# Kernel optimization log

Measured on AMD Instinct MI355X. Metric: run time of the kernel, lower is better.

Reference implementation:

```python
import jax, jax.numpy as jnp
import numpy as np

D_MODEL = 1024
NUM_HEADS = 16
HEAD_DIM = D_MODEL // NUM_HEADS  # 64
ROPE_THETA = 10000.0
BATCH = 2
SEQ = 2048
NEG_INF = -1e30


def setup_inputs() -> dict:
    key = jax.random.key(0)
    ks = jax.random.split(key, 6)
    std = 1.0 / np.sqrt(D_MODEL)
    x = jax.random.normal(ks[0], (BATCH, SEQ, D_MODEL), dtype=jnp.float32)
    wq = jax.random.normal(ks[1], (D_MODEL, D_MODEL), dtype=jnp.float32) * std
    wk = jax.random.normal(ks[2], (D_MODEL, D_MODEL), dtype=jnp.float32) * std
    wv = jax.random.normal(ks[3], (D_MODEL, D_MODEL), dtype=jnp.float32) * std
    wo = jax.random.normal(ks[4], (D_MODEL, D_MODEL), dtype=jnp.float32) * std
    token_positions = jnp.broadcast_to(jnp.arange(SEQ, dtype=jnp.int32)[None, :], (BATCH, SEQ))
    return {"x": x, "token_positions": token_positions, "wq": wq, "wk": wk, "wv": wv, "wo": wo}


def _apply_rope(t, token_positions):
    # t: (B, H, S, head_dim), token_positions: (B, S)
    half = HEAD_DIM // 2
    inv_freq = 1.0 / (ROPE_THETA ** (2.0 * jnp.arange(half, dtype=jnp.float32) / HEAD_DIM))
    angles = token_positions.astype(jnp.float32)[..., None] * inv_freq  # (B, S, half)
    cos = jnp.cos(angles)[:, None, :, :]  # (B, 1, S, half)
    sin = jnp.sin(angles)[:, None, :, :]
    tp = t.reshape(*t.shape[:-1], half, 2)  # interleaved pairs
    x1, x2 = tp[..., 0], tp[..., 1]
    r1 = x1 * cos - x2 * sin
    r2 = x1 * sin + x2 * cos
    return jnp.stack([r1, r2], axis=-1).reshape(t.shape)


def reference(x, token_positions, wq, wk, wv, wo):
    B, S, D = x.shape
    H, hd = NUM_HEADS, HEAD_DIM
    # projections (Linear: y = x @ W.T, no bias)
    q = (x @ wq.T).reshape(B, S, H, hd).transpose(0, 2, 1, 3)  # (B, H, S, hd)
    k = (x @ wk.T).reshape(B, S, H, hd).transpose(0, 2, 1, 3)
    v = (x @ wv.T).reshape(B, S, H, hd).transpose(0, 2, 1, 3)
    # RoPE on Q, K
    q = _apply_rope(q, token_positions)
    k = _apply_rope(k, token_positions)
    # causal scaled dot-product attention
    scores = jnp.einsum("bhqd,bhkd->bhqk", q, k) / jnp.sqrt(jnp.float32(hd))
    mask = jnp.tril(jnp.ones((S, S), dtype=bool))
    scores = jnp.where(mask, scores, NEG_INF)
    probs = jax.nn.softmax(scores, axis=-1)
    attn = jnp.einsum("bhqk,bhkd->bhqd", probs, v)  # (B, H, S, hd)
    attn = attn.transpose(0, 2, 1, 3).reshape(B, S, D)
    return attn @ wo.T
```

## Files before the change

kernel.cpp:

```cpp
#include <hip/hip_runtime.h>
#include <stdint.h>
#include <math.h>

#define SEQ 2048
#define NH 16
#define DM 1024

typedef __bf16 bf16x8 __attribute__((ext_vector_type(8)));
typedef __bf16 bf16x2 __attribute__((ext_vector_type(2)));
typedef short s16x4 __attribute__((ext_vector_type(4)));
typedef short s16x8 __attribute__((ext_vector_type(8)));
typedef float f32x4 __attribute__((ext_vector_type(4)));
typedef float f32x2 __attribute__((ext_vector_type(2)));

#define ASM_VMCNT0  asm volatile("s_waitcnt vmcnt(0)" ::: "memory")
#define ASM_BARRIER asm volatile("s_barrier" ::: "memory")

__device__ __forceinline__ unsigned short f2bf(float f) {
  union { float f; unsigned u; } v; v.f = f;
  unsigned r = v.u + 0x7fffu + ((v.u >> 16) & 1u);
  return (unsigned short)(r >> 16);
}
__device__ __forceinline__ unsigned pk2(float a, float b) {
  f32x2 v = {a, b};
  bf16x2 r = __builtin_convertvector(v, bf16x2);
  union { bf16x2 h; unsigned u; } c; c.h = r;
  return c.u;
}
__device__ __forceinline__ void load_lds16(const void* g, void* l) {
  __builtin_amdgcn_global_load_lds((__attribute__((address_space(1))) void*)g,
                                   (__attribute__((address_space(3))) void*)l,
                                   16, 0, 0);
}

__global__ void cvt_all(const float* __restrict__ x, const float* __restrict__ wq,
                        const float* __restrict__ wk, const float* __restrict__ wv,
                        const float* __restrict__ wo, unsigned short* __restrict__ ws) {
  const int i = blockIdx.x * blockDim.x + threadIdx.x;
  const int off = i * 4;
  const float* src;
  unsigned short* dst;
  if (off < 4194304) {
    src = x + off;  dst = ws + off;
  } else {
    const int r = off - 4194304;
    const int w = r >> 20, o = r & 1048575;
    const float* tabs[4] = {wq, wk, wv, wo};
    src = tabs[w] + o;  dst = ws + 4194304 + (w << 20) + o;
  }
  const float4 v = *(const float4*)src;
  uint2 u;
  u.x = pk2(v.x, v.y);
  u.y = pk2(v.z, v.w);
  *(uint2*)dst = u;
}

__launch_bounds__(256, 3)
__global__ void gemm_qkv(const unsigned short* __restrict__ X,
                         const unsigned short* __restrict__ W3,
                         unsigned short* __restrict__ Qr,
                         unsigned short* __restrict__ Kr,
                         unsigned short* __restrict__ Vt,
                         const int* __restrict__ tp) {
  __shared__ __align__(16) char smem[32768];

  const int t = threadIdx.x;
  const int lane = t & 63, wave = t >> 6;
  const int quad = lane >> 4, l16 = lane & 15;
  const int m0 = blockIdx.y * 128, n0 = blockIdx.x * 128;
  const int wm = (wave >> 1) * 64, wn = (wave & 1) * 64;

  f32x4 acc[4][4];
#pragma unroll
  for (int i = 0; i < 4; i++)
#pragma unroll
    for (int j = 0; j < 4; j++) { acc[i][j][0]=0.f; acc[i][j][1]=0.f; acc[i][j][2]=0.f; acc[i][j][3]=0.f; }

  const int rr = t >> 2;
  const int cc = (t & 3) * 8;

#define QKV_STAGE(bufidx, k0_) do {                                               \
    char* a_ = smem + (bufidx) * 8192;                                            \
    char* b_ = smem + 16384 + (bufidx) * 8192;                                    \
    _Pragma("unroll")                                                             \
    for (int i_ = 0; i_ < 2; i_++) {                                              \
      load_lds16(X  + (uint64_t)(m0 + i_ * 64 + rr) * 1024 + (k0_) + cc,          \
                 a_ + i_ * 4096 + wave * 1024);                                   \
      load_lds16(W3 + (uint64_t)(n0 + i_ * 64 + rr) * 1024 + (k0_) + cc,          \
                 b_ + i_ * 4096 + wave * 1024);                                   \
    }                                                                             \
  } while (0)

  QKV_STAGE(0, 0);

  for (int k0 = 0; k0 < 1024; k0 += 32) {
    const int buf = (k0 >> 5) & 1;
    ASM_VMCNT0;
    ASM_BARRIER;
    if (k0 + 32 < 1024) QKV_STAGE(buf ^ 1, k0 + 32);
    char* As = smem + buf * 8192;
    char* Bs = smem + 16384 + buf * 8192;

    bf16x8 af[4], bfr[4];
#pragma unroll
    for (int i = 0; i < 4; i++) {
      af[i]  = *(const bf16x8*)(As + (wm + i * 16 + l16) * 64 + quad * 16);
      bfr[i] = *(const bf16x8*)(Bs + (wn + i * 16 + l16) * 64 + quad * 16);
    }
#pragma unroll
    for (int i = 0; i < 4; i++)
#pragma unroll
      for (int j = 0; j < 4; j++)
        acc[i][j] = __builtin_amdgcn_mfma_f32_16x16x32_bf16(af[i], bfr[j], acc[i][j], 0, 0, 0);
  }
#undef QKV_STAGE

  if (n0 < 2048) {
    unsigned short* dst = (n0 < 1024) ? Qr : Kr;
    float fr[4]; int dd[4], hh[4];
#pragma unroll
    for (int j = 0; j < 4; j++) {
      const int n = n0 + wn + j * 16 + l16;
      dd[j] = n & 63;
      hh[j] = (n & 1023) >> 6;
      fr[j] = __builtin_amdgcn_exp2f(-0.20762050594f * (float)(dd[j] & ~1)) * 0.15915494309f;
    }
    const float sgnodd = (l16 & 1) ? 1.f : -1.f;
#pragma unroll
    for (int i = 0; i < 4; i++) {
#pragma unroll
      for (int r = 0; r < 4; r++) {
        const int m = m0 + wm + i * 16 + quad * 4 + r;
        const int s = m & 2047, b = m >> 11;
        const float posf = (float)tp[m];
#pragma unroll
        for (int j = 0; j < 4; j++) {
          const float v = acc[i][j][r];
          const float p = __shfl_xor(v, 1);
          float rev = posf * fr[j];
          rev -= floorf(rev);
          float sn, cs;
          asm("v_sin_f32 %0, %1" : "=v"(sn) : "v"(rev));
          asm("v_cos_f32 %0, %1" : "=v"(cs) : "v"(rev));
          const float rv = fmaf(v, cs, p * sn * sgnodd);
          dst[((uint64_t)((b * NH + hh[j]) * SEQ + s)) * 64 + dd[j]] = f2bf(rv);
        }
      }
    }
  } else {
#pragma unroll
    for (int i = 0; i < 4; i++) {
      const int m = m0 + wm + i * 16 + quad * 4;
      const int s = m & 2047, b = m >> 11;
      const int sl = s & 63;
      const int qv = (sl >> 2) & 3, nv = sl >> 4;
      const int g = (s & ~63) + qv * 16 + (nv >> 1) * 8 + (nv & 1) * 4;
#pragma unroll
      for (int j = 0; j < 4; j++) {
        const int n = n0 - 2048 + wn + j * 16 + l16;
        const int h = n >> 6, d = n & 63;
        uint2 w;
        w.x = pk2(acc[i][j][0], acc[i][j][1]);
        w.y = pk2(acc[i][j][2], acc[i][j][3]);
        *(uint2*)(Vt + ((uint64_t)((b * NH + h) * 64 + d)) * SEQ + g) = w;
      }
    }
  }
}

__launch_bounds__(256, 2)
__global__ void gemm_ao(const unsigned short* __restrict__ A,
                        const unsigned short* __restrict__ B,
                        float* __restrict__ C) {
  __shared__ __align__(16) char smem[32768];

  const int t = threadIdx.x;
  const int lane = t & 63, wave = t >> 6;
  const int quad = lane >> 4, l16 = lane & 15;
  const int m0 = blockIdx.y * 128, n0 = blockIdx.x * 128;
  const int wm = (wave >> 1) * 64, wn = (wave & 1) * 64;

  f32x4 acc[4][4];
#pragma unroll
  for (int i = 0; i < 4; i++)
#pragma unroll
    for (int j = 0; j < 4; j++) { acc[i][j][0]=0.f; acc[i][j][1]=0.f; acc[i][j][2]=0.f; acc[i][j][3]=0.f; }

  const int rr = t >> 2;
  const int cc = (t & 3) * 8;

#define AO_STAGE(bufidx, k0_) do {                                               \
    char* a_ = smem + (bufidx) * 8192;                                            \
    char* b_ = smem + 16384 + (bufidx) * 8192;                                    \
    _Pragma("unroll")                                                             \
    for (int i_ = 0; i_ < 2; i_++) {                                              \
      load_lds16(A + (uint64_t)(m0 + i_ * 64 + rr) * 1024 + (k0_) + cc,           \
                 a_ + i_ * 4096 + wave * 1024);                                   \
      load_lds16(B + (uint64_t)(n0 + i_ * 64 + rr) * 1024 + (k0_) + cc,           \
                 b_ + i_ * 4096 + wave * 1024);                                   \
    }                                                                             \
  } while (0)

  AO_STAGE(0, 0);

  for (int k0 = 0; k0 < 1024; k0 += 32) {
    const int buf = (k0 >> 5) & 1;
    ASM_VMCNT0;
    ASM_BARRIER;
    if (k0 + 32 < 1024) AO_STAGE(buf ^ 1, k0 + 32);
    char* As = smem + buf * 8192;
    char* Bs = smem + 16384 + buf * 8192;

    bf16x8 af[4], bfr[4];
#pragma unroll
    for (int i = 0; i < 4; i++) {
      af[i]  = *(const bf16x8*)(As + (wm + i * 16 + l16) * 64 + quad * 16);
      bfr[i] = *(const bf16x8*)(Bs + (wn + i * 16 + l16) * 64 + quad * 16);
    }
#pragma unroll
    for (int i = 0; i < 4; i++)
#pragma unroll
      for (int j = 0; j < 4; j++)
        acc[i][j] = __builtin_amdgcn_mfma_f32_16x16x32_bf16(af[i], bfr[j], acc[i][j], 0, 0, 0);
  }
#undef AO_STAGE

#pragma unroll
  for (int i = 0; i < 4; i++)
#pragma unroll
    for (int j = 0; j < 4; j++)
#pragma unroll
      for (int r = 0; r < 4; r++) {
        const int m = m0 + wm + i * 16 + quad * 4 + r;
        const int n = n0 + wn + j * 16 + l16;
        C[(uint64_t)m * DM + n] = acc[i][j][r];
      }
}

__launch_bounds__(512, 2)
__global__ void flash_attn(const unsigned short* __restrict__ Q,
                           const unsigned short* __restrict__ K,
                           const unsigned short* __restrict__ Vt,
                           unsigned short* __restrict__ Oa) {
  __shared__ __align__(16) char smem[32768];

  const int t = threadIdx.x;
  const int lane = t & 63, wave = t >> 6;
  const int quad = lane >> 4, l16 = lane & 15;
  const int lid = blockIdx.x;
  const int bh = lid & 31;
  const int a = lid >> 5;
  const uint64_t base = (uint64_t)bh * (SEQ * 64);
  const int qb0 = a * 128, qb1 = (15 - a) * 128;
  const int n0 = 2 * a + 2;
  const int qg0 = qb0 + wave * 16 + l16;
  const int qg1 = qb1 + wave * 16 + l16;
  const int b = bh >> 4, h = bh & 15;

  bf16x8 qf0[2], qf1[2];
  {
    const unsigned short* qp = Q + base + (uint64_t)qg0 * 64 + quad * 8;
    qf0[0] = *(const bf16x8*)qp;  qf0[1] = *(const bf16x8*)(qp + 32);
    const unsigned short* qq = Q + base + (uint64_t)qg1 * 64 + quad * 8;
    qf1[0] = *(const bf16x8*)qq;  qf1[1] = *(const bf16x8*)(qq + 32);
  }

  f32x4 o[4];
#pragma unroll
  for (int i = 0; i < 4; i++) { o[i][0]=0.f; o[i][1]=0.f; o[i][2]=0.f; o[i][3]=0.f; }
  float lI = 0.f;

  const int srow = wave * 8 + (lane >> 3);
  const int sc = ((lane & 7) ^ ((lane >> 3) & 7)) * 8;
  const int swz = (l16 & 7);

#define STAGE(bufidx, kb_) do {                                                   \
    load_lds16(K  + base + (uint64_t)((kb_) + srow) * 64 + sc,                    \
               smem + (bufidx) * 8192 + wave * 1024);                             \
    load_lds16(Vt + base + (uint64_t)srow * SEQ + (kb_) + sc,                     \
               smem + 16384 + (bufidx) * 8192 + wave * 1024);                     \
  } while (0)

  STAGE(0, 0);

  const float c1 = 0.18033688011f;

  for (int it = 0; it < 34; it++) {
    const bool ph1 = it >= n0;
    const int kb = (ph1 ? it - n0 : it) * 64;
    const int buf = it & 1;
    ASM_VMCNT0;
    ASM_BARRIER;
    if (it + 1 < 34) {
      const int itn = it + 1;
      const int kbn = ((itn >= n0) ? itn - n0 : itn) * 64;
      STAGE(buf ^ 1, kbn);
    }
    char* ks = smem + buf * 8192;
    char* vs = smem + 16384 + buf * 8192;

    const bf16x8* qf = ph1 ? qf1 : qf0;
    const int qg = ph1 ? qg1 : qg0;
    const int qb = ph1 ? qb1 : qb0;
    int nbmax = ((qb + wave * 16 + 15 - kb) >> 4) + 1;
    nbmax = nbmax > 4 ? 4 : (nbmax < 0 ? 0 : nbmax);
    const bool diag = (kb + 63) > (qb + wave * 16);

    f32x4 sf[4];
    float ls = 0.f;
#pragma unroll
    for (int nb = 0; nb < 4; nb++) {
      if (nb < nbmax) {
        f32x4 s; s[0]=0.f; s[1]=0.f; s[2]=0.f; s[3]=0.f;
#pragma unroll
        for (int kk = 0; kk < 2; kk++) {
          bf16x8 kfr = *(const bf16x8*)(ks + (nb * 16 + l16) * 128 + (((kk * 4 + quad) ^ swz) * 16));
          s = __builtin_amdgcn_mfma_f32_16x16x32_bf16(kfr, qf[kk], s, 0, 0, 0);
        }
        if (diag) {
#pragma unroll
          for (int r = 0; r < 4; r++) {
            const int key = kb + nb * 16 + quad * 4 + r;
            const float p = (key <= qg) ? __builtin_amdgcn_exp2f(s[r] * c1) : 0.f;
            sf[nb][r] = p;  ls += p;
          }
        } else {
#pragma unroll
          for (int r = 0; r < 4; r++) {
            const float p = __builtin_amdgcn_exp2f(s[r] * c1);
            sf[nb][r] = p;  ls += p;
          }
        }
      }
    }
    lI += ls;

#pragma unroll
    for (int np = 0; np < 2; np++) {
      if (2 * np < nbmax) {
        union { uint2 u; s16x4 h; } p0;
        p0.u.x = pk2(sf[2 * np][0], sf[2 * np][1]);
        p0.u.y = pk2(sf[2 * np][2], sf[2 * np][3]);
        const bool hi = (2 * np + 1 < nbmax);
        union { uint2 u; s16x4 h; } p1;
        if (hi) {
          p1.u.x = pk2(sf[2 * np + 1][0], sf[2 * np + 1][1]);
          p1.u.y = pk2(sf[2 * np + 1][2], sf[2 * np + 1][3]);
        }
#pragma unroll
        for (int db = 0; db < 4; db++) {
          s16x8 vv = *(const s16x8*)(vs + (db * 16 + l16) * 128 +
                                     (((quad * 2 + np) ^ swz) * 16));
          s16x4 vlo = __builtin_shufflevector(vv, vv, 0, 1, 2, 3);
          o[db] = __builtin_amdgcn_mfma_f32_16x16x16bf16_1k(vlo, p0.h, o[db], 0, 0, 0);
          if (hi) {
            s16x4 vhi = __builtin_shufflevector(vv, vv, 4, 5, 6, 7);
            o[db] = __builtin_amdgcn_mfma_f32_16x16x16bf16_1k(vhi, p1.h, o[db], 0, 0, 0);
          }
        }
      }
    }

    if (it == n0 - 1) {
      float lr = lI;
      lr += __shfl_xor(lr, 16);
      lr += __shfl_xor(lr, 32);
      const float invl = 1.0f / lr;
      unsigned short* orow = Oa + ((uint64_t)(b * SEQ + qg0)) * DM + h * 64 + quad * 4;
#pragma unroll
      for (int db = 0; db < 4; db++) {
        uint2 w;
        w.x = pk2(o[db][0] * invl, o[db][1] * invl);
        w.y = pk2(o[db][2] * invl, o[db][3] * invl);
        *(uint2*)(orow + db * 16) = w;
        o[db][0]=0.f; o[db][1]=0.f; o[db][2]=0.f; o[db][3]=0.f;
      }
      lI = 0.f;
    }
  }
#undef STAGE

  float lr = lI;
  lr += __shfl_xor(lr, 16);
  lr += __shfl_xor(lr, 32);
  const float invl = 1.0f / lr;
  unsigned short* orow = Oa + ((uint64_t)(b * SEQ + qg1)) * DM + h * 64 + quad * 4;
#pragma unroll
  for (int db = 0; db < 4; db++) {
    uint2 w;
    w.x = pk2(o[db][0] * invl, o[db][1] * invl);
    w.y = pk2(o[db][2] * invl, o[db][3] * invl);
    *(uint2*)(orow + db * 16) = w;
  }
}

extern "C" void kernel_launch(void* const* d_in, const int* in_sizes, int n_in,
                              void* d_out, int out_size, void* d_ws, size_t ws_size,
                              hipStream_t stream) {
  const float* x  = (const float*)d_in[0];
  const int* tp   = (const int*)d_in[1];
  const float* wq = (const float*)d_in[2];
  const float* wk = (const float*)d_in[3];
  const float* wv = (const float*)d_in[4];
  const float* wo = (const float*)d_in[5];
  float* out = (float*)d_out;

  unsigned short* ws = (unsigned short*)d_ws;
  unsigned short* xb  = ws;
  unsigned short* w3b = ws + 4194304;
  unsigned short* wob = ws + 7340032;
  unsigned short* Qr  = ws + 8388608;
  unsigned short* Kr  = ws + 12582912;
  unsigned short* Vt  = ws + 16777216;
  unsigned short* At  = ws + 20971520;

  cvt_all<<<8192, 256, 0, stream>>>(x, wq, wk, wv, wo, ws);
  gemm_qkv<<<dim3(24, 32), 256, 0, stream>>>(xb, w3b, Qr, Kr, Vt, tp);
  flash_attn<<<256, 512, 0, stream>>>(Qr, Kr, Vt, At);
  gemm_ao<<<dim3(8, 32), 256, 0, stream>>>(At, wob, out);
}
```

Before: 178.3 us.

## Split waves into two groups processing paired causal q-tiles concurrently

After: 183.0 us. 1.03x slower.

```diff
diff --git a/kernel.cpp b/kernel.cpp
--- a/kernel.cpp
+++ b/kernel.cpp
@@ -242,156 +242,165 @@
                            const unsigned short* __restrict__ K,
                            const unsigned short* __restrict__ Vt,
                            unsigned short* __restrict__ Oa) {
-  __shared__ __align__(16) char smem[32768];
+  __shared__ __align__(16) char smem[65536];
 
   const int t = threadIdx.x;
   const int lane = t & 63, wave = t >> 6;
   const int quad = lane >> 4, l16 = lane & 15;
+  const int g = wave >> 2, wv = wave & 3;
   const int lid = blockIdx.x;
   const int bh = lid & 31;
   const int a = lid >> 5;
   const uint64_t base = (uint64_t)bh * (SEQ * 64);
-  const int qb0 = a * 128, qb1 = (15 - a) * 128;
-  const int n0 = 2 * a + 2;
-  const int qg0 = qb0 + wave * 16 + l16;
-  const int qg1 = qb1 + wave * 16 + l16;
+  const int qb = (g ? (15 - a) : a) * 128;
+  const int ng0 = 2 * a + 2, ng1 = 32 - 2 * a;
+  const int ngMy = g ? ng1 : ng0;
+  const int qlo = qb + wv * 32;
+  const int qg0 = qlo + l16;
+  const int qg1 = qlo + 16 + l16;
   const int b = bh >> 4, h = bh & 15;
 
-  bf16x8 qf0[2], qf1[2];
+  bf16x8 qf[2][2];
   {
-    const unsigned short* qp = Q + base + (uint64_t)qg0 * 64 + quad * 8;
-    qf0[0] = *(const bf16x8*)qp;  qf0[1] = *(const bf16x8*)(qp + 32);
-    const unsigned short* qq = Q + base + (uint64_t)qg1 * 64 + quad * 8;
-    qf1[0] = *(const bf16x8*)qq;  qf1[1] = *(const bf16x8*)(qq + 32);
-  }
-
-  f32x4 o[4];
-#pragma unroll
-  for (int i = 0; i < 4; i++) { o[i][0]=0.f; o[i][1]=0.f; o[i][2]=0.f; o[i][3]=0.f; }
-  float lI = 0.f;
+    const unsigned short* qp0 = Q + base + (uint64_t)qg0 * 64 + quad * 8;
+    qf[0][0] = *(const bf16x8*)qp0;  qf[0][1] = *(const bf16x8*)(qp0 + 32);
+    const unsigned short* qp1 = Q + base + (uint64_t)qg1 * 64 + quad * 8;
+    qf[1][0] = *(const bf16x8*)qp1;  qf[1][1] = *(const bf16x8*)(qp1 + 32);
+  }
+
+  f32x4 o0[4], o1[4];
+#pragma unroll
+  for (int i = 0; i < 4; i++) {
+    o0[i][0]=0.f; o0[i][1]=0.f; o0[i][2]=0.f; o0[i][3]=0.f;
+    o1[i][0]=0.f; o1[i][1]=0.f; o1[i][2]=0.f; o1[i][3]=0.f;
+  }
+  float lI0 = 0.f, lI1 = 0.f;
 
   const int srow = wave * 8 + (lane >> 3);
   const int sc = ((lane & 7) ^ ((lane >> 3) & 7)) * 8;
   const int swz = (l16 & 7);
 
-#define STAGE(bufidx, kb_) do {                                                   \
+#define STAGE(gg, bufidx, kb_) do {                                               \
     load_lds16(K  + base + (uint64_t)((kb_) + srow) * 64 + sc,                    \
-               smem + (bufidx) * 8192 + wave * 1024);                             \
+               smem + (gg) * 32768 + (bufidx) * 16384 + wave * 1024);             \
     load_lds16(Vt + base + (uint64_t)srow * SEQ + (kb_) + sc,                     \
-               smem + 16384 + (bufidx) * 8192 + wave * 1024);                     \
+               smem + (gg) * 32768 + (bufidx) * 16384 + 8192 + wave * 1024);      \
   } while (0)
 
-  STAGE(0, 0);
+  STAGE(0, 0, 0);
+  STAGE(1, 0, 0);
 
   const float c1 = 0.18033688011f;
-
-  for (int it = 0; it < 34; it++) {
-    const bool ph1 = it >= n0;
-    const int kb = (ph1 ? it - n0 : it) * 64;
+  const int nIt = ng1;
+
+  for (int it = 0; it < nIt; it++) {
     const int buf = it & 1;
     ASM_VMCNT0;
     ASM_BARRIER;
-    if (it + 1 < 34) {
-      const int itn = it + 1;
-      const int kbn = ((itn >= n0) ? itn - n0 : itn) * 64;
-      STAGE(buf ^ 1, kbn);
-    }
-    char* ks = smem + buf * 8192;
-    char* vs = smem + 16384 + buf * 8192;
-
-    const bf16x8* qf = ph1 ? qf1 : qf0;
-    const int qg = ph1 ? qg1 : qg0;
-    const int qb = ph1 ? qb1 : qb0;
-    int nbmax = ((qb + wave * 16 + 15 - kb) >> 4) + 1;
-    nbmax = nbmax > 4 ? 4 : (nbmax < 0 ? 0 : nbmax);
-    const bool diag = (kb + 63) > (qb + wave * 16);
-
-    f32x4 sf[4];
-    float ls = 0.f;
-#pragma unroll
-    for (int nb = 0; nb < 4; nb++) {
-      if (nb < nbmax) {
-        f32x4 s; s[0]=0.f; s[1]=0.f; s[2]=0.f; s[3]=0.f;
-#pragma unroll
-        for (int kk = 0; kk < 2; kk++) {
-          bf16x8 kfr = *(const bf16x8*)(ks + (nb * 16 + l16) * 128 + (((kk * 4 + quad) ^ swz) * 16));
-          s = __builtin_amdgcn_mfma_f32_16x16x32_bf16(kfr, qf[kk], s, 0, 0, 0);
-        }
-        if (diag) {
-#pragma unroll
-          for (int r = 0; r < 4; r++) {
-            const int key = kb + nb * 16 + quad * 4 + r;
-            const float p = (key <= qg) ? __builtin_amdgcn_exp2f(s[r] * c1) : 0.f;
-            sf[nb][r] = p;  ls += p;
+    const int itn = it + 1;
+    if (itn < ng0) STAGE(0, itn & 1, itn * 64);
+    if (itn < ng1) STAGE(1, itn & 1, itn * 64);
+
+    if (it < ngMy) {
+      const int kb = it * 64;
+      char* ks = smem + g * 32768 + buf * 16384;
+      char* vs = ks + 8192;
+
+      int nbmax = ((qlo + 31 - kb) >> 4) + 1;
+      nbmax = nbmax > 4 ? 4 : (nbmax < 0 ? 0 : nbmax);
+      const bool diag = (kb + 63) > qlo;
+
+      f32x4 sf0[4], sf1[4];
+      float ls0 = 0.f, ls1 = 0.f;
+#pragma unroll
+      for (int nb = 0; nb < 4; nb++) {
+        if (nb < nbmax) {
+          f32x4 s0; s0[0]=0.f; s0[1]=0.f; s0[2]=0.f; s0[3]=0.f;
+          f32x4 s1; s1[0]=0.f; s1[1]=0.f; s1[2]=0.f; s1[3]=0.f;
+#pragma unroll
+          for (int kk = 0; kk < 2; kk++) {
+            bf16x8 kfr = *(const bf16x8*)(ks + (nb * 16 + l16) * 128 + (((kk * 4 + quad) ^ swz) * 16));
+            s0 = __builtin_amdgcn_mfma_f32_16x16x32_bf16(kfr, qf[0][kk], s0, 0, 0, 0);
+            s1 = __builtin_amdgcn_mfma_f32_16x16x32_bf16(kfr, qf[1][kk], s1, 0, 0, 0);
           }
-        } else {
-#pragma unroll
-          for (int r = 0; r < 4; r++) {
-            const float p = __builtin_amdgcn_exp2f(s[r] * c1);
-            sf[nb][r] = p;  ls += p;
+          if (diag) {
+#pragma unroll
+            for (int r = 0; r < 4; r++) {
+              const int key = kb + nb * 16 + quad * 4 + r;
+              const float p0 = (key <= qg0) ? __builtin_amdgcn_exp2f(s0[r] * c1) : 0.f;
+              sf0[nb][r] = p0;  ls0 += p0;
+              const float p1 = (key <= qg1) ? __builtin_amdgcn_exp2f(s1[r] * c1) : 0.f;
+              sf1[nb][r] = p1;  ls1 += p1;
+            }
+          } else {
+#pragma unroll
+            for (int r = 0; r < 4; r++) {
+              const float p0 = __builtin_amdgcn_exp2f(s0[r] * c1);
+              sf0[nb][r] = p0;  ls0 += p0;
+              const float p1 = __builtin_amdgcn_exp2f(s1[r] * c1);
+              sf1[nb][r] = p1;  ls1 += p1;
+            }
           }
         }
       }
-    }
-    lI += ls;
-
-#pragma unroll
-    for (int np = 0; np < 2; np++) {
-      if (2 * np < nbmax) {
-        union { uint2 u; s16x4 h; } p0;
-        p0.u.x = pk2(sf[2 * np][0], sf[2 * np][1]);
-        p0.u.y = pk2(sf[2 * np][2], sf[2 * np][3]);
-        const bool hi = (2 * np + 1 < nbmax);
-        union { uint2 u; s16x4 h; } p1;
-        if (hi) {
-          p1.u.x = pk2(sf[2 * np + 1][0], sf[2 * np + 1][1]);
-          p1.u.y = pk2(sf[2 * np + 1][2], sf[2 * np + 1][3]);
-        }
-#pragma unroll
-        for (int db = 0; db < 4; db++) {
-          s16x8 vv = *(const s16x8*)(vs + (db * 16 + l16) * 128 +
-                                     (((quad * 2 + np) ^ swz) * 16));
-          s16x4 vlo = __builtin_shufflevector(vv, vv, 0, 1, 2, 3);
-          o[db] = __builtin_amdgcn_mfma_f32_16x16x16bf16_1k(vlo, p0.h, o[db], 0, 0, 0);
+      lI0 += ls0;  lI1 += ls1;
+
+#pragma unroll
+      for (int np = 0; np < 2; np++) {
+        if (2 * np < nbmax) {
+          union { uint2 u; s16x4 h; } a0, b0, a1, b1;
+          a0.u.x = pk2(sf0[2 * np][0], sf0[2 * np][1]);
+          a0.u.y = pk2(sf0[2 * np][2], sf0[2 * np][3]);
+          b0.u.x = pk2(sf1[2 * np][0], sf1[2 * np][1]);
+          b0.u.y = pk2(sf1[2 * np][2], sf1[2 * np][3]);
+          const bool hi = (2 * np + 1 < nbmax);
           if (hi) {
-            s16x4 vhi = __builtin_shufflevector(vv, vv, 4, 5, 6, 7);
-            o[db] = __builtin_amdgcn_mfma_f32_16x16x16bf16_1k(vhi, p1.h, o[db], 0, 0, 0);
+            a1.u.x = pk2(sf0[2 * np + 1][0], sf0[2 * np + 1][1]);
+            a1.u.y = pk2(sf0[2 * np + 1][2], sf0[2 * np + 1][3]);
+            b1.u.x = pk2(sf1[2 * np + 1][0], sf1[2 * np + 1][1]);
+            b1.u.y = pk2(sf1[2 * np + 1][2], sf1[2 * np + 1][3]);
+          }
+#pragma unroll
+          for (int db = 0; db < 4; db++) {
+            s16x8 vv = *(const s16x8*)(vs + (db * 16 + l16) * 128 +
+                                       (((quad * 2 + np) ^ swz) * 16));
+            s16x4 vlo = __builtin_shufflevector(vv, vv, 0, 1, 2, 3);
+            o0[db] = __builtin_amdgcn_mfma_f32_16x16x16bf16_1k(vlo, a0.h, o0[db], 0, 0, 0);
+            o1[db] = __builtin_amdgcn_mfma_f32_16x16x16bf16_1k(vlo, b0.h, o1[db], 0, 0, 0);
+            if (hi) {
+              s16x4 vhi = __builtin_shufflevector(vv, vv, 4, 5, 6, 7);
+              o0[db] = __builtin_amdgcn_mfma_f32_16x16x16bf16_1k(vhi, a1.h, o0[db], 0, 0, 0);
+              o1[db] = __builtin_amdgcn_mfma_f32_16x16x16bf16_1k(vhi, b1.h, o1[db], 0, 0, 0);
+            }
           }
         }
       }
-    }
-
-    if (it == n0 - 1) {
-      float lr = lI;
-      lr += __shfl_xor(lr, 16);
-      lr += __shfl_xor(lr, 32);
-      const float invl = 1.0f / lr;
-      unsigned short* orow = Oa + ((uint64_t)(b * SEQ + qg0)) * DM + h * 64 + quad * 4;
-#pragma unroll
-      for (int db = 0; db < 4; db++) {
-        uint2 w;
-        w.x = pk2(o[db][0] * invl, o[db][1] * invl);
-        w.y = pk2(o[db][2] * invl, o[db][3] * invl);
-        *(uint2*)(orow + db * 16) = w;
-        o[db][0]=0.f; o[db][1]=0.f; o[db][2]=0.f; o[db][3]=0.f;
-      }
-      lI = 0.f;
+
+      if (it == ngMy - 1) {
+        float lr0 = lI0;
+        lr0 += __shfl_xor(lr0, 16);
+        lr0 += __shfl_xor(lr0, 32);
+        const float il0 = 1.0f / lr0;
+        float lr1 = lI1;
+        lr1 += __shfl_xor(lr1, 16);
+        lr1 += __shfl_xor(lr1, 32);
+        const float il1 = 1.0f / lr1;
+        unsigned short* p0r = Oa + ((uint64_t)(b * SEQ + qg0)) * DM + h * 64 + quad * 4;
+        unsigned short* p1r = Oa + ((uint64_t)(b * SEQ + qg1)) * DM + h * 64 + quad * 4;
+#pragma unroll
+        for (int db = 0; db < 4; db++) {
+          uint2 w;
+          w.x = pk2(o0[db][0] * il0, o0[db][1] * il0);
+          w.y = pk2(o0[db][2] * il0, o0[db][3] * il0);
+          *(uint2*)(p0r + db * 16) = w;
+          w.x = pk2(o1[db][0] * il1, o1[db][1] * il1);
+          w.y = pk2(o1[db][2] * il1, o1[db][3] * il1);
+          *(uint2*)(p1r + db * 16) = w;
+        }
+      }
     }
   }
 #undef STAGE
-
-  float lr = lI;
-  lr += __shfl_xor(lr, 16);
-  lr += __shfl_xor(lr, 32);
-  const float invl = 1.0f / lr;
-  unsigned short* orow = Oa + ((uint64_t)(b * SEQ + qg1)) * DM + h * 64 + quad * 4;
-#pragma unroll
-  for (int db = 0; db < 4; db++) {
-    uint2 w;
-    w.x = pk2(o[db][0] * invl, o[db][1] * invl);
-    w.y = pk2(o[db][2] * invl, o[db][3] * invl);
-    *(uint2*)(orow + db * 16) = w;
-  }
 }
 
 extern "C" void kernel_launch(void* const* d_in, const int* in_sizes, int n_in,
```

## Split flash attention into 64-row query tiles, heaviest-first, with 256-thread blocks

Applied to the files above, without the earlier changes.

After: 174.2 us. -2.3%, faster.

```diff
diff --git a/kernel.cpp b/kernel.cpp
--- a/kernel.cpp
+++ b/kernel.cpp
@@ -237,7 +237,7 @@
       }
 }
 
-__launch_bounds__(512, 2)
+__launch_bounds__(256, 4)
 __global__ void flash_attn(const unsigned short* __restrict__ Q,
                            const unsigned short* __restrict__ K,
                            const unsigned short* __restrict__ Vt,
@@ -245,24 +245,21 @@
   __shared__ __align__(16) char smem[32768];
 
   const int t = threadIdx.x;
-  const int lane = t & 63, wave = t >> 6;
+  const int lane = t & 63, wid = t >> 6;
   const int quad = lane >> 4, l16 = lane & 15;
-  const int lid = blockIdx.x;
-  const int bh = lid & 31;
-  const int a = lid >> 5;
+  const int u = blockIdx.x;
+  const int tq = 31 - (u >> 5);
+  const int bh = u & 31;
   const uint64_t base = (uint64_t)bh * (SEQ * 64);
-  const int qb0 = a * 128, qb1 = (15 - a) * 128;
-  const int n0 = 2 * a + 2;
-  const int qg0 = qb0 + wave * 16 + l16;
-  const int qg1 = qb1 + wave * 16 + l16;
+  const int qb = tq * 64;
+  const int ng = tq + 1;
+  const int qg = qb + wid * 16 + l16;
   const int b = bh >> 4, h = bh & 15;
 
-  bf16x8 qf0[2], qf1[2];
+  bf16x8 qf[2];
   {
-    const unsigned short* qp = Q + base + (uint64_t)qg0 * 64 + quad * 8;
-    qf0[0] = *(const bf16x8*)qp;  qf0[1] = *(const bf16x8*)(qp + 32);
-    const unsigned short* qq = Q + base + (uint64_t)qg1 * 64 + quad * 8;
-    qf1[0] = *(const bf16x8*)qq;  qf1[1] = *(const bf16x8*)(qq + 32);
+    const unsigned short* qp = Q + base + (uint64_t)qg * 64 + quad * 8;
+    qf[0] = *(const bf16x8*)qp;  qf[1] = *(const bf16x8*)(qp + 32);
   }
 
   f32x4 o[4];
@@ -270,41 +267,37 @@
   for (int i = 0; i < 4; i++) { o[i][0]=0.f; o[i][1]=0.f; o[i][2]=0.f; o[i][3]=0.f; }
   float lI = 0.f;
 
-  const int srow = wave * 8 + (lane >> 3);
-  const int sc = ((lane & 7) ^ ((lane >> 3) & 7)) * 8;
+  const int sr8 = lane >> 3;
+  const int sc = ((lane & 7) ^ sr8) * 8;
   const int swz = (l16 & 7);
 
 #define STAGE(bufidx, kb_) do {                                                   \
-    load_lds16(K  + base + (uint64_t)((kb_) + srow) * 64 + sc,                    \
-               smem + (bufidx) * 8192 + wave * 1024);                             \
-    load_lds16(Vt + base + (uint64_t)srow * SEQ + (kb_) + sc,                     \
-               smem + 16384 + (bufidx) * 8192 + wave * 1024);                     \
+    _Pragma("unroll")                                                             \
+    for (int i_ = 0; i_ < 2; i_++) {                                              \
+      const int r_ = wid * 16 + i_ * 8 + sr8;                                     \
+      load_lds16(K  + base + (uint64_t)((kb_) + r_) * 64 + sc,                    \
+                 smem + (bufidx) * 8192 + wid * 2048 + i_ * 1024);                \
+      load_lds16(Vt + base + (uint64_t)r_ * SEQ + (kb_) + sc,                     \
+                 smem + 16384 + (bufidx) * 8192 + wid * 2048 + i_ * 1024);        \
+    }                                                                             \
   } while (0)
 
   STAGE(0, 0);
 
   const float c1 = 0.18033688011f;
 
-  for (int it = 0; it < 34; it++) {
-    const bool ph1 = it >= n0;
-    const int kb = (ph1 ? it - n0 : it) * 64;
+  for (int it = 0; it < ng; it++) {
+    const int kb = it * 64;
     const int buf = it & 1;
     ASM_VMCNT0;
     ASM_BARRIER;
-    if (it + 1 < 34) {
-      const int itn = it + 1;
-      const int kbn = ((itn >= n0) ? itn - n0 : itn) * 64;
-      STAGE(buf ^ 1, kbn);
-    }
+    if (it + 1 < ng) STAGE(buf ^ 1, (it + 1) * 64);
     char* ks = smem + buf * 8192;
     char* vs = smem + 16384 + buf * 8192;
 
-    const bf16x8* qf = ph1 ? qf1 : qf0;
-    const int qg = ph1 ? qg1 : qg0;
-    const int qb = ph1 ? qb1 : qb0;
-    int nbmax = ((qb + wave * 16 + 15 - kb) >> 4) + 1;
+    int nbmax = ((qb + wid * 16 + 15 - kb) >> 4) + 1;
     nbmax = nbmax > 4 ? 4 : (nbmax < 0 ? 0 : nbmax);
-    const bool diag = (kb + 63) > (qb + wave * 16);
+    const bool diag = (kb + 63) > (qb + wid * 16);
 
     f32x4 sf[4];
     float ls = 0.f;
@@ -360,23 +353,6 @@
         }
       }
     }
-
-    if (it == n0 - 1) {
-      float lr = lI;
-      lr += __shfl_xor(lr, 16);
-      lr += __shfl_xor(lr, 32);
-      const float invl = 1.0f / lr;
-      unsigned short* orow = Oa + ((uint64_t)(b * SEQ + qg0)) * DM + h * 64 + quad * 4;
-#pragma unroll
-      for (int db = 0; db < 4; db++) {
-        uint2 w;
-        w.x = pk2(o[db][0] * invl, o[db][1] * invl);
-        w.y = pk2(o[db][2] * invl, o[db][3] * invl);
-        *(uint2*)(orow + db * 16) = w;
-        o[db][0]=0.f; o[db][1]=0.f; o[db][2]=0.f; o[db][3]=0.f;
-      }
-      lI = 0.f;
-    }
   }
 #undef STAGE
 
@@ -384,7 +360,7 @@
   lr += __shfl_xor(lr, 16);
   lr += __shfl_xor(lr, 32);
   const float invl = 1.0f / lr;
-  unsigned short* orow = Oa + ((uint64_t)(b * SEQ + qg1)) * DM + h * 64 + quad * 4;
+  unsigned short* orow = Oa + ((uint64_t)(b * SEQ + qg)) * DM + h * 64 + quad * 4;
 #pragma unroll
   for (int db = 0; db < 4; db++) {
     uint2 w;
@@ -416,6 +392,6 @@
 
   cvt_all<<<8192, 256, 0, stream>>>(x, wq, wk, wv, wo, ws);
   gemm_qkv<<<dim3(24, 32), 256, 0, stream>>>(xb, w3b, Qr, Kr, Vt, tp);
-  flash_attn<<<256, 512, 0, stream>>>(Qr, Kr, Vt, At);
+  flash_attn<<<1024, 256, 0, stream>>>(Qr, Kr, Vt, At);
   gemm_ao<<<dim3(8, 32), 256, 0, stream>>>(At, wob, out);
 }
```
